# Performance work log

Hardware: AMD Instinct MI355X
Metric: run time of the kernel (lower is better)

The kernel has to match this reference:

```python
import jax, jax.numpy as jnp
import numpy as np

N = 150000   # nonempty octree nodes at this depth
CIN = 256
CB = 64      # bottleneck channels = out_channels / bottleneck
COUT = 256
G = 32       # group-norm groups
K = 27       # 3x3x3 neighborhood
EPS = 1e-5


def group_norm(x, gamma, beta, groups=G):
    # x: [N, C]; octree GN treats the N nodes as the spatial extent of one instance
    n, c = x.shape
    xg = x.reshape(n, groups, c // groups)
    mu = xg.mean(axis=(0, 2), keepdims=True)
    var = xg.var(axis=(0, 2), keepdims=True)
    xg = (xg - mu) * jax.lax.rsqrt(var + EPS)
    return xg.reshape(n, c) * gamma + beta


def setup_inputs() -> dict:
    key = jax.random.key(0)
    ks = jax.random.split(key, 5)
    return {
        "data": jax.random.normal(ks[0], (N, CIN), jnp.float32),
        "neigh": jax.random.randint(ks[1], (N, K), 0, N, jnp.int32),
        "w1a": jax.random.normal(ks[2], (CIN, CB), jnp.float32) * 0.05,
        "g1a": jnp.ones((CB,), jnp.float32),
        "b1a": jnp.zeros((CB,), jnp.float32),
        "w3": jax.random.normal(ks[3], (K, CB, CB), jnp.float32) * 0.05,
        "g3": jnp.ones((CB,), jnp.float32),
        "b3": jnp.zeros((CB,), jnp.float32),
        "w1b": jax.random.normal(ks[4], (CB, COUT), jnp.float32) * 0.05,
        "g1b": jnp.ones((COUT,), jnp.float32),
        "b1b": jnp.zeros((COUT,), jnp.float32),
    }


def reference(data, neigh, w1a, g1a, b1a, w3, g3, b3, w1b, g1b, b1b):
    # conv1x1a + GN + ReLU
    x = jax.nn.relu(group_norm(data @ w1a, g1a, b1a))
    # octree 3x3x3 sparse conv: gather 27 neighbors, GEMM against [27,CB,CB] kernel
    gathered = x[neigh]                      # [N, 27, CB]
    y = jnp.einsum('nkc,kcd->nd', gathered, w3)
    y = jax.nn.relu(group_norm(y, g3, b3))
    # conv1x1b + GN
    z = group_norm(y @ w1b, g1b, b1b)
    # residual add (in_channels == out_channels -> identity skip) + ReLU
    return jax.nn.relu(z + data)
```

## Files before the change

kernel.cpp:

```cpp
#include <hip/hip_runtime.h>
#include <math.h>

#define CIN 256
#define CB 64
#define COUT 256
#define KNB 27
#define EPS 1e-5f

typedef unsigned short u16;
typedef __attribute__((ext_vector_type(8))) short short8;
typedef __attribute__((ext_vector_type(4))) float f32x4;

__device__ inline short f2bf(float f) {
    union { float f; unsigned u; } v; v.f = f;
    unsigned r = v.u + 0x7fff + ((v.u >> 16) & 1);
    return (short)(r >> 16);
}
__device__ inline float bf2f(short s) {
    union { unsigned u; float f; } v; v.u = ((unsigned)(u16)s) << 16;
    return v.f;
}
__device__ inline short8 pack8(float4 x0, float4 x1) {
    short8 r;
    r[0] = f2bf(x0.x); r[1] = f2bf(x0.y); r[2] = f2bf(x0.z); r[3] = f2bf(x0.w);
    r[4] = f2bf(x1.x); r[5] = f2bf(x1.y); r[6] = f2bf(x1.z); r[7] = f2bf(x1.w);
    return r;
}

__global__ void k_prep(const float* __restrict__ w1a, const float* __restrict__ w3,
                       const float* __restrict__ w1b, u16* __restrict__ w1at,
                       u16* __restrict__ w3img, u16* __restrict__ w1bt)
{
    int i = blockIdx.x * 256 + threadIdx.x;
    if (i < 16384) {
        int k = i >> 6, d = i & 63;
        w1at[d * 256 + k] = (u16)f2bf(w1a[i]);
    } else if (i < 126976) {
        int j = i - 16384;
        int k = j >> 12, c = (j >> 6) & 63, d = j & 63;
        w3img[(size_t)k * 4096 + d * 64 + (c ^ ((d & 7) << 3))] = (u16)f2bf(w3[j]);
    } else if (i < 143360) {
        int j = i - 126976;
        int c = j >> 8, d = j & 255;
        w1bt[d * 64 + c] = (u16)f2bf(w1b[j]);
    }
}

__global__ __launch_bounds__(256) void k_gemm1(const float* __restrict__ data,
        const u16* __restrict__ w1at, u16* __restrict__ t1,
        float* __restrict__ stats, int n)
{
    __shared__ float s_sum[32], s_sq[32];
    const int tid = threadIdx.x;
    if (tid < 32) { s_sum[tid] = 0.f; s_sq[tid] = 0.f; }
    __syncthreads();
    const int l = tid & 63, wv = tid >> 6;
    const int ll = l & 15, lh = l >> 4;
    const int rowbase = blockIdx.x * 256 + wv * 64;

    f32x4 acc[4][4] = {};
#pragma unroll
    for (int kc = 0; kc < 8; ++kc) {
        short8 b[4];
#pragma unroll
        for (int f = 0; f < 4; ++f)
            b[f] = *(const short8*)(w1at + (size_t)(f * 16 + ll) * 256 + kc * 32 + lh * 8);
#pragma unroll
        for (int rt = 0; rt < 4; ++rt) {
            int row = rowbase + rt * 16 + ll;
            int rowc = (row < n) ? row : 0;
            const float* ar = data + (size_t)rowc * CIN + kc * 32 + lh * 8;
            short8 a = pack8(*(const float4*)ar, *(const float4*)(ar + 4));
#pragma unroll
            for (int f = 0; f < 4; ++f)
                acc[rt][f] = __builtin_amdgcn_mfma_f32_16x16x32_bf16(a, b[f], acc[rt][f], 0, 0, 0);
        }
    }
    float gs[4] = {0.f, 0.f, 0.f, 0.f}, gq[4] = {0.f, 0.f, 0.f, 0.f};
#pragma unroll
    for (int rt = 0; rt < 4; ++rt) {
#pragma unroll
        for (int f = 0; f < 4; ++f) {
#pragma unroll
            for (int r = 0; r < 4; ++r) {
                int rr = rowbase + rt * 16 + lh * 4 + r;
                if (rr < n) {
                    float v = acc[rt][f][r];
                    t1[(size_t)rr * CB + f * 16 + ll] = (u16)f2bf(v);
                    gs[f] += v; gq[f] += v * v;
                }
            }
        }
    }
#pragma unroll
    for (int f = 0; f < 4; ++f) {
        float s = gs[f], q = gq[f];
        s += __shfl_xor(s, 1); s += __shfl_xor(s, 16); s += __shfl_xor(s, 32);
        q += __shfl_xor(q, 1); q += __shfl_xor(q, 16); q += __shfl_xor(q, 32);
        if ((l & 0x31) == 0) {
            atomicAdd(&s_sum[f * 8 + (ll >> 1)], s);
            atomicAdd(&s_sq [f * 8 + (ll >> 1)], q);
        }
    }
    __syncthreads();
    if (tid < 32) {
        atomicAdd(&stats[tid], s_sum[tid]);
        atomicAdd(&stats[32 + tid], s_sq[tid]);
    }
}

__global__ void k_apply64(u16* __restrict__ buf, const float* __restrict__ st,
        const float* __restrict__ gamma, const float* __restrict__ beta, int n)
{
    const float cnt = (float)n * 2.0f;
    const int total = n * 8;
    for (int i = blockIdx.x * blockDim.x + threadIdx.x; i < total;
         i += gridDim.x * blockDim.x) {
        int c0 = (i & 7) * 8;
        short8 v = ((short8*)buf)[i];
#pragma unroll
        for (int j = 0; j < 8; ++j) {
            int c = c0 + j, g = c >> 1;
            float mu = st[g] / cnt;
            float var = st[32 + g] / cnt - mu * mu;
            float inv = rsqrtf(var + EPS);
            float x = bf2f(v[j]);
            x = fmaxf((x - mu) * inv * gamma[c] + beta[c], 0.f);
            v[j] = f2bf(x);
        }
        ((short8*)buf)[i] = v;
    }
}

__global__ __launch_bounds__(256) void k_conv(const u16* __restrict__ xb,
        const int* __restrict__ neigh, const u16* __restrict__ w3img,
        u16* __restrict__ y, float* __restrict__ stats, int n)
{
    __shared__ u16 s_w3[2][4096];
    __shared__ int s_idx[64 * KNB];
    __shared__ float s_sum[32], s_sq[32];
    const int tid = threadIdx.x;
    if (tid < 32) { s_sum[tid] = 0.f; s_sq[tid] = 0.f; }
    const int row0 = blockIdx.x * 64;
    for (int j = tid; j < 64 * KNB; j += 256) {
        int node = row0 + j / KNB;
        s_idx[j] = (node < n) ? neigh[(size_t)row0 * KNB + j] : 0;
    }
    const int l = tid & 63, wv = tid >> 6;
    const int ll = l & 15, lh = l >> 4;
    const int node27 = (wv * 16 + ll) * KNB;

    {
        const short8* src = (const short8*)(w3img);
        short8 v0 = src[tid * 2], v1 = src[tid * 2 + 1];
        ((short8*)&s_w3[0][0])[tid * 2] = v0;
        ((short8*)&s_w3[0][0])[tid * 2 + 1] = v1;
    }
    __syncthreads();
    short8 a0c, a1c;
    {
        int idx = s_idx[node27];
        const u16* xr = xb + (size_t)idx * CB + lh * 8;
        a0c = *(const short8*)(xr);
        a1c = *(const short8*)(xr + 32);
    }

    f32x4 acc[4] = {};
    for (int k = 0; k < KNB; ++k) {
        const int cur = k & 1;
        short8 a0n, a1n;
        if (k + 1 < KNB) {
            const short8* src = (const short8*)(w3img + (size_t)(k + 1) * 4096);
            short8 v0 = src[tid * 2], v1 = src[tid * 2 + 1];
            ((short8*)&s_w3[cur ^ 1][0])[tid * 2] = v0;
            ((short8*)&s_w3[cur ^ 1][0])[tid * 2 + 1] = v1;
            int idx = s_idx[node27 + k + 1];
            const u16* xr = xb + (size_t)idx * CB + lh * 8;
            a0n = *(const short8*)(xr);
            a1n = *(const short8*)(xr + 32);
        }
#pragma unroll
        for (int f = 0; f < 4; ++f) {
            int d = f * 16 + ll;
            int swz = (d & 7) << 4;
            short8 b0 = *(const short8*)((const char*)&s_w3[cur][0] + d * 128 + ((lh * 16) ^ swz));
            short8 b1 = *(const short8*)((const char*)&s_w3[cur][0] + d * 128 + ((64 + lh * 16) ^ swz));
            acc[f] = __builtin_amdgcn_mfma_f32_16x16x32_bf16(a0c, b0, acc[f], 0, 0, 0);
            acc[f] = __builtin_amdgcn_mfma_f32_16x16x32_bf16(a1c, b1, acc[f], 0, 0, 0);
        }
        __syncthreads();
        a0c = a0n; a1c = a1n;
    }
    float gs[4] = {0.f, 0.f, 0.f, 0.f}, gq[4] = {0.f, 0.f, 0.f, 0.f};
#pragma unroll
    for (int f = 0; f < 4; ++f) {
#pragma unroll
        for (int r = 0; r < 4; ++r) {
            int rr = row0 + wv * 16 + lh * 4 + r;
            if (rr < n) {
                float v = acc[f][r];
                y[(size_t)rr * CB + f * 16 + ll] = (u16)f2bf(v);
                gs[f] += v; gq[f] += v * v;
            }
        }
    }
#pragma unroll
    for (int f = 0; f < 4; ++f) {
        float s = gs[f], q = gq[f];
        s += __shfl_xor(s, 1); s += __shfl_xor(s, 16); s += __shfl_xor(s, 32);
        q += __shfl_xor(q, 1); q += __shfl_xor(q, 16); q += __shfl_xor(q, 32);
        if ((l & 0x31) == 0) {
            atomicAdd(&s_sum[f * 8 + (ll >> 1)], s);
            atomicAdd(&s_sq [f * 8 + (ll >> 1)], q);
        }
    }
    __syncthreads();
    if (tid < 32) {
        atomicAdd(&stats[64 + tid], s_sum[tid]);
        atomicAdd(&stats[96 + tid], s_sq[tid]);
    }
}

__global__ __launch_bounds__(256) void k_gemm2(const u16* __restrict__ y2,
        const u16* __restrict__ w1bt, float* __restrict__ z,
        float* __restrict__ stats, int n)
{
    __shared__ float s_sum[8], s_sq[8];
    const int tid = threadIdx.x;
    if (tid < 8) { s_sum[tid] = 0.f; s_sq[tid] = 0.f; }
    __syncthreads();
    const int l = tid & 63, wv = tid >> 6;
    const int ll = l & 15, lh = l >> 4;
    const int rowbase = blockIdx.x * 256 + wv * 64;
    const int cb = blockIdx.y;

    short8 b0[4], b1[4];
#pragma unroll
    for (int f = 0; f < 4; ++f) {
        const u16* br = w1bt + (size_t)(cb * 64 + f * 16 + ll) * CB + lh * 8;
        b0[f] = *(const short8*)(br);
        b1[f] = *(const short8*)(br + 32);
    }
    f32x4 acc[4][4] = {};
#pragma unroll
    for (int rt = 0; rt < 4; ++rt) {
        int row = rowbase + rt * 16 + ll;
        int rowc = (row < n) ? row : 0;
        const u16* ar = y2 + (size_t)rowc * CB + lh * 8;
        short8 a0 = *(const short8*)(ar);
        short8 a1 = *(const short8*)(ar + 32);
#pragma unroll
        for (int f = 0; f < 4; ++f) {
            acc[rt][f] = __builtin_amdgcn_mfma_f32_16x16x32_bf16(a0, b0[f], acc[rt][f], 0, 0, 0);
            acc[rt][f] = __builtin_amdgcn_mfma_f32_16x16x32_bf16(a1, b1[f], acc[rt][f], 0, 0, 0);
        }
    }
    float gs[4] = {0.f, 0.f, 0.f, 0.f}, gq[4] = {0.f, 0.f, 0.f, 0.f};
#pragma unroll
    for (int rt = 0; rt < 4; ++rt) {
#pragma unroll
        for (int f = 0; f < 4; ++f) {
#pragma unroll
            for (int r = 0; r < 4; ++r) {
                int rr = rowbase + rt * 16 + lh * 4 + r;
                if (rr < n) {
                    float v = acc[rt][f][r];
                    z[(size_t)rr * COUT + cb * 64 + f * 16 + ll] = v;
                    gs[f] += v; gq[f] += v * v;
                }
            }
        }
    }
#pragma unroll
    for (int f = 0; f < 4; ++f) {
        float s = gs[f], q = gq[f];
        s += __shfl_xor(s, 1); s += __shfl_xor(s, 2); s += __shfl_xor(s, 4);
        s += __shfl_xor(s, 16); s += __shfl_xor(s, 32);
        q += __shfl_xor(q, 1); q += __shfl_xor(q, 2); q += __shfl_xor(q, 4);
        q += __shfl_xor(q, 16); q += __shfl_xor(q, 32);
        if ((l & 0x37) == 0) {
            atomicAdd(&s_sum[f * 2 + (ll >> 3)], s);
            atomicAdd(&s_sq [f * 2 + (ll >> 3)], q);
        }
    }
    __syncthreads();
    if (tid < 8) {
        atomicAdd(&stats[128 + cb * 8 + tid], s_sum[tid]);
        atomicAdd(&stats[160 + cb * 8 + tid], s_sq[tid]);
    }
}

__global__ void k_final(float* __restrict__ zo, const float* __restrict__ data,
        const float* __restrict__ st, const float* __restrict__ gamma,
        const float* __restrict__ beta, int n)
{
    const float cnt = (float)n * 8.0f;
    const int total = n * (COUT / 4);
    for (int i = blockIdx.x * blockDim.x + threadIdx.x; i < total;
         i += gridDim.x * blockDim.x) {
        int c4 = (i & (COUT / 4 - 1)) * 4;
        int g = c4 >> 3;
        float mu = st[g] / cnt;
        float var = st[32 + g] / cnt - mu * mu;
        float inv = rsqrtf(var + EPS);
        float4 zv = *(float4*)(zo + (size_t)i * 4);
        float4 dv = *(const float4*)(data + (size_t)i * 4);
        zv.x = fmaxf((zv.x - mu) * inv * gamma[c4 + 0] + beta[c4 + 0] + dv.x, 0.f);
        zv.y = fmaxf((zv.y - mu) * inv * gamma[c4 + 1] + beta[c4 + 1] + dv.y, 0.f);
        zv.z = fmaxf((zv.z - mu) * inv * gamma[c4 + 2] + beta[c4 + 2] + dv.z, 0.f);
        zv.w = fmaxf((zv.w - mu) * inv * gamma[c4 + 3] + beta[c4 + 3] + dv.w, 0.f);
        *(float4*)(zo + (size_t)i * 4) = zv;
    }
}

extern "C" void kernel_launch(void* const* d_in, const int* in_sizes, int n_in,
                              void* d_out, int out_size, void* d_ws, size_t ws_size,
                              hipStream_t stream)
{
    const float* data = (const float*)d_in[0];
    const int*   neigh = (const int*)d_in[1];
    const float* w1a = (const float*)d_in[2];
    const float* g1a = (const float*)d_in[3];
    const float* b1a = (const float*)d_in[4];
    const float* w3  = (const float*)d_in[5];
    const float* g3  = (const float*)d_in[6];
    const float* b3  = (const float*)d_in[7];
    const float* w1b = (const float*)d_in[8];
    const float* g1b = (const float*)d_in[9];
    const float* b1b = (const float*)d_in[10];
    float* out = (float*)d_out;
    float* ws  = (float*)d_ws;

    const int n = in_sizes[0] / CIN;

    float* stats = ws;
    u16* w1at  = (u16*)(ws + 256);
    u16* w3img = w1at + 16384;
    u16* w1bt  = w3img + 110592;
    u16* t1    = w1bt + 16384;
    u16* ybuf  = t1 + (size_t)n * CB;

    hipMemsetAsync(stats, 0, 192 * sizeof(float), stream);

    const int nb64  = (n + 63) / 64;
    const int nb256 = (n + 255) / 256;
    k_prep<<<560, 256, 0, stream>>>(w1a, w3, w1b, w1at, w3img, w1bt);
    k_gemm1<<<nb256, 256, 0, stream>>>(data, w1at, t1, stats, n);
    k_apply64<<<2048, 256, 0, stream>>>(t1, stats, g1a, b1a, n);
    k_conv<<<nb64, 256, 0, stream>>>(t1, neigh, w3img, ybuf, stats, n);
    k_apply64<<<2048, 256, 0, stream>>>(ybuf, stats + 64, g3, b3, n);
    k_gemm2<<<dim3(nb256, 4), 256, 0, stream>>>(ybuf, w1bt, out, stats, n);
    k_final<<<2048, 256, 0, stream>>>(out, data, stats + 128, g1b, b1b, n);
}
```

Measured before the change: 315.5 us.

## Double conv rows per block and store gemm2 output as bf16 intermediate

The sparse conv kernel now processes 128 nodes per block with two row tiles per wave. Each LDS weight slice is reused across twice as many MFMAs, and the per-k weight load and sync are amortized. The conv also moves the LDS store of the next weight slice after the MFMAs and sets a launch-bounds occupancy hint. Separately, gemm2 writes z as bf16 into workspace when it is large enough, and a new final kernel reads the bf16 z, which cuts intermediate traffic at some precision cost.

```diff
diff --git a/kernel.cpp b/kernel.cpp
--- a/kernel.cpp
+++ b/kernel.cpp
@@ -132,23 +132,22 @@
     }
 }
 
-__global__ __launch_bounds__(256) void k_conv(const u16* __restrict__ xb,
+__global__ __launch_bounds__(256, 4) void k_conv(const u16* __restrict__ xb,
         const int* __restrict__ neigh, const u16* __restrict__ w3img,
         u16* __restrict__ y, float* __restrict__ stats, int n)
 {
     __shared__ u16 s_w3[2][4096];
-    __shared__ int s_idx[64 * KNB];
+    __shared__ int s_idx[128 * KNB];
     __shared__ float s_sum[32], s_sq[32];
     const int tid = threadIdx.x;
     if (tid < 32) { s_sum[tid] = 0.f; s_sq[tid] = 0.f; }
-    const int row0 = blockIdx.x * 64;
-    for (int j = tid; j < 64 * KNB; j += 256) {
+    const int row0 = blockIdx.x * 128;
+    for (int j = tid; j < 128 * KNB; j += 256) {
         int node = row0 + j / KNB;
         s_idx[j] = (node < n) ? neigh[(size_t)row0 * KNB + j] : 0;
     }
     const int l = tid & 63, wv = tid >> 6;
     const int ll = l & 15, lh = l >> 4;
-    const int node27 = (wv * 16 + ll) * KNB;
 
     {
         const short8* src = (const short8*)(w3img);
@@ -157,27 +156,32 @@
         ((short8*)&s_w3[0][0])[tid * 2 + 1] = v1;
     }
     __syncthreads();
-    short8 a0c, a1c;
-    {
-        int idx = s_idx[node27];
+    short8 a0c[2], a1c[2];
+#pragma unroll
+    for (int rt = 0; rt < 2; ++rt) {
+        int idx = s_idx[(wv * 32 + rt * 16 + ll) * KNB];
         const u16* xr = xb + (size_t)idx * CB + lh * 8;
-        a0c = *(const short8*)(xr);
-        a1c = *(const short8*)(xr + 32);
-    }
-
-    f32x4 acc[4] = {};
+        a0c[rt] = *(const short8*)(xr);
+        a1c[rt] = *(const short8*)(xr + 32);
+    }
+
+    f32x4 acc[2][4] = {};
     for (int k = 0; k < KNB; ++k) {
         const int cur = k & 1;
-        short8 a0n, a1n;
-        if (k + 1 < KNB) {
+        const bool more = (k + 1 < KNB);
+        short8 w0, w1;
+        short8 a0n[2], a1n[2];
+        if (more) {
             const short8* src = (const short8*)(w3img + (size_t)(k + 1) * 4096);
-            short8 v0 = src[tid * 2], v1 = src[tid * 2 + 1];
-            ((short8*)&s_w3[cur ^ 1][0])[tid * 2] = v0;
-            ((short8*)&s_w3[cur ^ 1][0])[tid * 2 + 1] = v1;
-            int idx = s_idx[node27 + k + 1];
-            const u16* xr = xb + (size_t)idx * CB + lh * 8;
-            a0n = *(const short8*)(xr);
-            a1n = *(const short8*)(xr + 32);
+            w0 = src[tid * 2];
+            w1 = src[tid * 2 + 1];
+#pragma unroll
+            for (int rt = 0; rt < 2; ++rt) {
+                int idx = s_idx[(wv * 32 + rt * 16 + ll) * KNB + k + 1];
+                const u16* xr = xb + (size_t)idx * CB + lh * 8;
+                a0n[rt] = *(const short8*)(xr);
+                a1n[rt] = *(const short8*)(xr + 32);
+            }
         }
 #pragma unroll
         for (int f = 0; f < 4; ++f) {
@@ -185,22 +189,33 @@
             int swz = (d & 7) << 4;
             short8 b0 = *(const short8*)((const char*)&s_w3[cur][0] + d * 128 + ((lh * 16) ^ swz));
             short8 b1 = *(const short8*)((const char*)&s_w3[cur][0] + d * 128 + ((64 + lh * 16) ^ swz));
-            acc[f] = __builtin_amdgcn_mfma_f32_16x16x32_bf16(a0c, b0, acc[f], 0, 0, 0);
-            acc[f] = __builtin_amdgcn_mfma_f32_16x16x32_bf16(a1c, b1, acc[f], 0, 0, 0);
+#pragma unroll
+            for (int rt = 0; rt < 2; ++rt) {
+                acc[rt][f] = __builtin_amdgcn_mfma_f32_16x16x32_bf16(a0c[rt], b0, acc[rt][f], 0, 0, 0);
+                acc[rt][f] = __builtin_amdgcn_mfma_f32_16x16x32_bf16(a1c[rt], b1, acc[rt][f], 0, 0, 0);
+            }
+        }
+        if (more) {
+            ((short8*)&s_w3[cur ^ 1][0])[tid * 2] = w0;
+            ((short8*)&s_w3[cur ^ 1][0])[tid * 2 + 1] = w1;
+#pragma unroll
+            for (int rt = 0; rt < 2; ++rt) { a0c[rt] = a0n[rt]; a1c[rt] = a1n[rt]; }
         }
         __syncthreads();
-        a0c = a0n; a1c = a1n;
     }
     float gs[4] = {0.f, 0.f, 0.f, 0.f}, gq[4] = {0.f, 0.f, 0.f, 0.f};
 #pragma unroll
-    for (int f = 0; f < 4; ++f) {
-#pragma unroll
-        for (int r = 0; r < 4; ++r) {
-            int rr = row0 + wv * 16 + lh * 4 + r;
-            if (rr < n) {
-                float v = acc[f][r];
-                y[(size_t)rr * CB + f * 16 + ll] = (u16)f2bf(v);
-                gs[f] += v; gq[f] += v * v;
+    for (int rt = 0; rt < 2; ++rt) {
+#pragma unroll
+        for (int f = 0; f < 4; ++f) {
+#pragma unroll
+            for (int r = 0; r < 4; ++r) {
+                int rr = row0 + wv * 32 + rt * 16 + lh * 4 + r;
+                if (rr < n) {
+                    float v = acc[rt][f][r];
+                    y[(size_t)rr * CB + f * 16 + ll] = (u16)f2bf(v);
+                    gs[f] += v; gq[f] += v * v;
+                }
             }
         }
     }
@@ -222,7 +237,7 @@
 }
 
 __global__ __launch_bounds__(256) void k_gemm2(const u16* __restrict__ y2,
-        const u16* __restrict__ w1bt, float* __restrict__ z,
+        const u16* __restrict__ w1bt, float* __restrict__ z, u16* __restrict__ zb,
         float* __restrict__ stats, int n)
 {
     __shared__ float s_sum[8], s_sq[8];
@@ -265,7 +280,8 @@
                 int rr = rowbase + rt * 16 + lh * 4 + r;
                 if (rr < n) {
                     float v = acc[rt][f][r];
-                    z[(size_t)rr * COUT + cb * 64 + f * 16 + ll] = v;
+                    size_t off = (size_t)rr * COUT + cb * 64 + f * 16 + ll;
+                    if (zb) zb[off] = (u16)f2bf(v); else z[off] = v;
                     gs[f] += v; gq[f] += v * v;
                 }
             }
@@ -287,6 +303,31 @@
     if (tid < 8) {
         atomicAdd(&stats[128 + cb * 8 + tid], s_sum[tid]);
         atomicAdd(&stats[160 + cb * 8 + tid], s_sq[tid]);
+    }
+}
+
+__global__ void k_final_bf(float* __restrict__ out, const u16* __restrict__ zb,
+        const float* __restrict__ data, const float* __restrict__ st,
+        const float* __restrict__ gamma, const float* __restrict__ beta, int n)
+{
+    const float cnt = (float)n * 8.0f;
+    const int total = n * 32;
+    for (int i = blockIdx.x * blockDim.x + threadIdx.x; i < total;
+         i += gridDim.x * blockDim.x) {
+        int c0 = (i & 31) * 8;
+        int g = c0 >> 3;
+        float mu = st[g] / cnt;
+        float var = st[32 + g] / cnt - mu * mu;
+        float inv = rsqrtf(var + EPS);
+        short8 zv = ((const short8*)zb)[i];
+        float dd[8], oo[8];
+        *(float4*)dd = *(const float4*)(data + (size_t)i * 8);
+        *(float4*)(dd + 4) = *(const float4*)(data + (size_t)i * 8 + 4);
+#pragma unroll
+        for (int j = 0; j < 8; ++j)
+            oo[j] = fmaxf((bf2f(zv[j]) - mu) * inv * gamma[c0 + j] + beta[c0 + j] + dd[j], 0.f);
+        *(float4*)(out + (size_t)i * 8) = *(float4*)oo;
+        *(float4*)(out + (size_t)i * 8 + 4) = *(float4*)(oo + 4);
     }
 }
 
@@ -339,16 +380,24 @@
     u16* w1bt  = w3img + 110592;
     u16* t1    = w1bt + 16384;
     u16* ybuf  = t1 + (size_t)n * CB;
+    u16* zb    = nullptr;
+    {
+        size_t need = 1024 + 286720 + (size_t)n * CB * 4 + (size_t)n * COUT * 2;
+        if (ws_size >= need) zb = ybuf + (size_t)n * CB;
+    }
 
     hipMemsetAsync(stats, 0, 192 * sizeof(float), stream);
 
-    const int nb64  = (n + 63) / 64;
+    const int nb128 = (n + 127) / 128;
     const int nb256 = (n + 255) / 256;
     k_prep<<<560, 256, 0, stream>>>(w1a, w3, w1b, w1at, w3img, w1bt);
     k_gemm1<<<nb256, 256, 0, stream>>>(data, w1at, t1, stats, n);
     k_apply64<<<2048, 256, 0, stream>>>(t1, stats, g1a, b1a, n);
-    k_conv<<<nb64, 256, 0, stream>>>(t1, neigh, w3img, ybuf, stats, n);
+    k_conv<<<nb128, 256, 0, stream>>>(t1, neigh, w3img, ybuf, stats, n);
     k_apply64<<<2048, 256, 0, stream>>>(ybuf, stats + 64, g3, b3, n);
-    k_gemm2<<<dim3(nb256, 4), 256, 0, stream>>>(ybuf, w1bt, out, stats, n);
-    k_final<<<2048, 256, 0, stream>>>(out, data, stats + 128, g1b, b1b, n);
-}
+    k_gemm2<<<dim3(nb256, 4), 256, 0, stream>>>(ybuf, w1bt, out, zb, stats, n);
+    if (zb)
+        k_final_bf<<<2048, 256, 0, stream>>>(out, zb, data, stats + 128, g1b, b1b, n);
+    else
+        k_final<<<2048, 256, 0, stream>>>(out, data, stats + 128, g1b, b1b, n);
+}
```

Result: faster. 296.4 us (-6.0%).
